# Kernel tuning notes

Hardware: AMD Instinct MI355X
Metric: run time of the kernel (lower is better)

Reference implementation:

```python
import jax, jax.numpy as jnp
import numpy as np

ALPHA = 0.2  # LeakyReLU negative slope


def _gat_layer(h, dst, adj, w, a_in, a_out, b):
    # h: [N, F_in], dst: [N, K] int (edge (i,k): i -> dst[i,k]), adj: [N, K]
    hid = h @ w                      # [N, D]
    s_in = hid @ a_in                # [N]  (attention applied to source-node half)
    s_out = hid @ a_out              # [N]  (attention applied to dest-node half)
    # edge scores, grouped per source node (matches view(-1, num_neighs) softmax)
    e = jax.nn.leaky_relu(s_in[:, None] + s_out[dst], ALPHA)   # [N, K]
    # torch code detaches attention (Variable(..., requires_grad=False))
    att = jax.lax.stop_gradient(jax.nn.softmax(e, axis=1))     # [N, K]
    w_edge = adj * att                                          # [N, K]
    # SpMM: out[i] = sum_k w_edge[i,k] * hid[dst[i,k]]
    out = jnp.einsum('nk,nkd->nd', w_edge, hid[dst]) + b        # [N, D]
    return out


def setup_inputs() -> dict:
    key = jax.random.key(0)
    ks = jax.random.split(key, 12)
    N, K, F, H, O = 100000, 16, 128, 128, 128
    stdv1 = 1.0 / np.sqrt(H)
    stdv2 = 1.0 / np.sqrt(O)
    u = lambda k, shp, s: jax.random.uniform(k, shp, jnp.float32, -s, s)
    return {
        'x': jax.random.normal(ks[0], (N, F), jnp.float32),
        'dst_idx': jax.random.randint(ks[1], (N, K), 0, N),
        'adj_vals': jax.random.uniform(ks[2], (N, K), jnp.float32),
        'w1': u(ks[3], (F, H), stdv1),
        'a_in1': jax.random.normal(ks[4], (H,), jnp.float32) * (1.414 / np.sqrt(H)),
        'a_out1': jax.random.normal(ks[5], (H,), jnp.float32) * (1.414 / np.sqrt(H)),
        'b1': u(ks[6], (H,), stdv1),
        'w2': u(ks[7], (H, O), stdv2),
        'a_in2': jax.random.normal(ks[8], (O,), jnp.float32) * (1.414 / np.sqrt(O)),
        'a_out2': jax.random.normal(ks[9], (O,), jnp.float32) * (1.414 / np.sqrt(O)),
        'b2': u(ks[10], (O,), stdv2),
    }


def reference(x, dst_idx, adj_vals, w1, a_in1, a_out1, b1, w2, a_in2, a_out2, b2):
    h = jax.nn.relu(_gat_layer(x, dst_idx, adj_vals, w1, a_in1, a_out1, b1))
    h = jax.nn.relu(_gat_layer(h, dst_idx, adj_vals, w2, a_in2, a_out2, b2))
    return h
```

## Files before the change

kernel.cpp:

```cpp
#include <hip/hip_runtime.h>

#define ALPHA 0.2f
#define LDA 136

typedef short bf16x8 __attribute__((ext_vector_type(8)));
typedef float f32x4  __attribute__((ext_vector_type(4)));

static __device__ __forceinline__ float bf2f(unsigned short u) {
    union { unsigned int i; float f; } v; v.i = ((unsigned int)u) << 16; return v.f;
}
static __device__ __forceinline__ unsigned short f2bf(float f) {
    union { float f; unsigned int i; } v; v.f = f;
    unsigned int x = v.i;
    return (unsigned short)((x + 0x7fffu + ((x >> 16) & 1u)) >> 16);
}

__global__ __launch_bounds__(128)
void prep_wT_kernel(const float* __restrict__ w1, const float* __restrict__ w2,
                    unsigned short* __restrict__ wT1, unsigned short* __restrict__ wT2)
{
    const int b = blockIdx.x;
    const float* w = (b >> 4) ? w2 : w1;
    unsigned short* wT = (b >> 4) ? wT2 : wT1;
    const int k0 = (b & 15) * 8;
    const int c = threadIdx.x;

    ushort4 u0, u1;
    u0.x = f2bf(w[(k0 + 0) * 128 + c]); u0.y = f2bf(w[(k0 + 1) * 128 + c]);
    u0.z = f2bf(w[(k0 + 2) * 128 + c]); u0.w = f2bf(w[(k0 + 3) * 128 + c]);
    u1.x = f2bf(w[(k0 + 4) * 128 + c]); u1.y = f2bf(w[(k0 + 5) * 128 + c]);
    u1.z = f2bf(w[(k0 + 6) * 128 + c]); u1.w = f2bf(w[(k0 + 7) * 128 + c]);
    *(ushort4*)&wT[c * 128 + k0]     = u0;
    *(ushort4*)&wT[c * 128 + k0 + 4] = u1;
}

__global__ __launch_bounds__(256, 4)
void gemm_score_mfma(const float* __restrict__ src,
                     const unsigned short* __restrict__ wT,
                     const float* __restrict__ a_in,
                     const float* __restrict__ a_out,
                     unsigned short* __restrict__ hid,
                     float* __restrict__ s_in,
                     float* __restrict__ s_out,
                     int n)
{
    __shared__ short Bs[128 * LDA];
    __shared__ float aS[2][128];

    const int tid  = threadIdx.x;
    const int lane = tid & 63;
    const int wv   = tid >> 6;
    const int m    = lane & 15;
    const int q    = lane >> 4;
    const int rbase = blockIdx.x * 64;
    const int row   = rbase + wv * 16 + m;
    const bool rok  = (row < n);

    if (tid < 128) { aS[0][tid] = a_in[tid]; aS[1][tid] = a_out[tid]; }

    bf16x8 aF[4];
    {
        const float* p = &src[(size_t)row * 128 + q * 8];
        #pragma unroll
        for (int ks = 0; ks < 4; ks++) {
            if (rok) {
                float4 v0 = *(const float4*)(p + ks * 32);
                float4 v1 = *(const float4*)(p + ks * 32 + 4);
                bf16x8 a;
                a[0] = (short)f2bf(v0.x); a[1] = (short)f2bf(v0.y);
                a[2] = (short)f2bf(v0.z); a[3] = (short)f2bf(v0.w);
                a[4] = (short)f2bf(v1.x); a[5] = (short)f2bf(v1.y);
                a[6] = (short)f2bf(v1.z); a[7] = (short)f2bf(v1.w);
                aF[ks] = a;
            } else aF[ks] = (bf16x8){0,0,0,0,0,0,0,0};
        }
    }

    #pragma unroll
    for (int i = 0; i < 8; i++) {
        int e = tid + i * 256;
        int nr = e >> 4, j = (e & 15) * 8;
        int4 v = *(const int4*)&wT[nr * 128 + j];
        *(int4*)&Bs[nr * LDA + j] = v;
    }
    __syncthreads();

    f32x4 acc[8];
    #pragma unroll
    for (int t = 0; t < 8; t++) acc[t] = (f32x4){0.f, 0.f, 0.f, 0.f};

    const short* Bbase = &Bs[m * LDA + q * 8];
    #pragma unroll
    for (int ks = 0; ks < 4; ks++) {
        #pragma unroll
        for (int t = 0; t < 8; t++) {
            bf16x8 bF = *(const bf16x8*)(Bbase + t * 16 * LDA + ks * 32);
            acc[t] = __builtin_amdgcn_mfma_f32_16x16x32_bf16(aF[ks], bF, acc[t], 0, 0, 0);
        }
    }

    float pin[4] = {0.f, 0.f, 0.f, 0.f}, pout[4] = {0.f, 0.f, 0.f, 0.f};
    #pragma unroll
    for (int t = 0; t < 8; t++) {
        float ai = aS[0][t * 16 + m];
        float ao = aS[1][t * 16 + m];
        #pragma unroll
        for (int r = 0; r < 4; r++) {
            pin[r]  += acc[t][r] * ai;
            pout[r] += acc[t][r] * ao;
        }
    }
    #pragma unroll
    for (int msk = 8; msk >= 1; msk >>= 1) {
        #pragma unroll
        for (int r = 0; r < 4; r++) {
            pin[r]  += __shfl_xor(pin[r],  msk);
            pout[r] += __shfl_xor(pout[r], msk);
        }
    }
    if (m == 0) {
        #pragma unroll
        for (int r = 0; r < 4; r++) {
            int g = rbase + wv * 16 + q * 4 + r;
            if (g < n) { s_in[g] = pin[r]; s_out[g] = pout[r]; }
        }
    }

    __syncthreads();
    short* Es = Bs;
    #pragma unroll
    for (int t = 0; t < 8; t++)
        #pragma unroll
        for (int r = 0; r < 4; r++)
            Es[(wv * 16 + q * 4 + r) * LDA + t * 16 + m] = (short)f2bf(acc[t][r]);
    __syncthreads();
    #pragma unroll
    for (int i = 0; i < 4; i++) {
        int e = tid + i * 256;
        int r = e >> 4, j = (e & 15) * 8;
        int gr = rbase + r;
        if (gr < n) {
            int4 v = *(const int4*)&Es[r * LDA + j];
            *(int4*)&hid[(size_t)gr * 128 + j] = v;
        }
    }
}

__global__ __launch_bounds__(256, 4)
void fused_agg_gemm(const unsigned short* __restrict__ hid1,
                    const float* __restrict__ s_in1,
                    const float* __restrict__ s_out1,
                    const int* __restrict__ dst,
                    const float* __restrict__ adj,
                    const float* __restrict__ bias1,
                    const unsigned short* __restrict__ wT2,
                    const float* __restrict__ a_in2,
                    const float* __restrict__ a_out2,
                    unsigned short* __restrict__ hid2,
                    float* __restrict__ s_in2,
                    float* __restrict__ s_out2,
                    int n)
{
    __shared__ short As[64 * LDA];
    __shared__ short Bs[64 * LDA];
    __shared__ float aS[2][128];

    const int tid  = threadIdx.x;
    const int lane = tid & 63;
    const int wv   = tid >> 6;
    const int rbase = blockIdx.x * 64;

    if (tid < 128) { aS[0][tid] = a_in2[tid]; aS[1][tid] = a_out2[tid]; }

    #pragma unroll
    for (int i = 0; i < 4; i++) {
        int e = tid + i * 256;
        int nr = e >> 4, j = (e & 15) * 8;
        int4 v = *(const int4*)&wT2[nr * 128 + j];
        *(int4*)&Bs[nr * LDA + j] = v;
    }

    const int jn  = lane >> 2;
    const int kq  = lane & 3;
    const int node = rbase + wv * 16 + jn;
    const bool nok = (node < n);

    int4   dk4 = make_int4(0, 0, 0, 0);
    float4 av4 = make_float4(0.f, 0.f, 0.f, 0.f);
    float  si  = 0.f;
    if (nok) {
        dk4 = *(const int4*)&dst[node * 16 + kq * 4];
        av4 = *(const float4*)&adj[node * 16 + kq * 4];
        si  = s_in1[node];
    }
    float e0 = si + s_out1[dk4.x], e1 = si + s_out1[dk4.y];
    float e2 = si + s_out1[dk4.z], e3 = si + s_out1[dk4.w];
    e0 = (e0 > 0.f) ? e0 : ALPHA * e0;  e1 = (e1 > 0.f) ? e1 : ALPHA * e1;
    e2 = (e2 > 0.f) ? e2 : ALPHA * e2;  e3 = (e3 > 0.f) ? e3 : ALPHA * e3;
    float mx = fmaxf(fmaxf(e0, e1), fmaxf(e2, e3));
    mx = fmaxf(mx, __shfl_xor(mx, 1));
    mx = fmaxf(mx, __shfl_xor(mx, 2));
    float p0 = __expf(e0 - mx), p1 = __expf(e1 - mx);
    float p2 = __expf(e2 - mx), p3 = __expf(e3 - mx);
    float sm = p0 + p1 + p2 + p3;
    sm += __shfl_xor(sm, 1);
    sm += __shfl_xor(sm, 2);
    const float inv = __frcp_rn(sm);
    float4 wk4 = make_float4(av4.x * p0 * inv, av4.y * p1 * inv,
                             av4.z * p2 * inv, av4.w * p3 * inv);

    const int c = lane * 2;
    const float2 bia = *(const float2*)&bias1[c];

    for (int j2 = 0; j2 < 16; j2++) {
        float accx = 0.f, accy = 0.f;
        #pragma unroll
        for (int k = 0; k < 16; k++) {
            const int srcl = j2 * 4 + (k >> 2);
            int   sdk, swki;
            if ((k & 3) == 0) { sdk = __builtin_amdgcn_readlane(dk4.x, srcl);
                                swki = __builtin_amdgcn_readlane(__float_as_int(wk4.x), srcl); }
            else if ((k & 3) == 1) { sdk = __builtin_amdgcn_readlane(dk4.y, srcl);
                                swki = __builtin_amdgcn_readlane(__float_as_int(wk4.y), srcl); }
            else if ((k & 3) == 2) { sdk = __builtin_amdgcn_readlane(dk4.z, srcl);
                                swki = __builtin_amdgcn_readlane(__float_as_int(wk4.z), srcl); }
            else             { sdk = __builtin_amdgcn_readlane(dk4.w, srcl);
                                swki = __builtin_amdgcn_readlane(__float_as_int(wk4.w), srcl); }
            float swk = __int_as_float(swki);
            ushort2 hq = *(const ushort2*)&hid1[(size_t)sdk * 128 + c];
            accx += swk * bf2f(hq.x);
            accy += swk * bf2f(hq.y);
        }
        float ox = fmaxf(accx + bia.x, 0.f);
        float oy = fmaxf(accy + bia.y, 0.f);
        ushort2 hv; hv.x = f2bf(ox); hv.y = f2bf(oy);
        *(ushort2*)&As[(wv * 16 + j2) * LDA + c] = hv;
    }
    __syncthreads();

    const int m = lane & 15;
    const int q = lane >> 4;

    bf16x8 aF[4];
    {
        const short* Abase = &As[(wv * 16 + m) * LDA + q * 8];
        #pragma unroll
        for (int ks = 0; ks < 4; ks++)
            aF[ks] = *(const bf16x8*)(Abase + ks * 32);
    }

    f32x4 acc[8];
    #pragma unroll
    for (int t = 0; t < 8; t++) acc[t] = (f32x4){0.f, 0.f, 0.f, 0.f};

    const short* Bbase = &Bs[m * LDA + q * 8];
    #pragma unroll
    for (int ks = 0; ks < 4; ks++) {
        #pragma unroll
        for (int t = 0; t < 4; t++) {
            bf16x8 bF = *(const bf16x8*)(Bbase + t * 16 * LDA + ks * 32);
            acc[t] = __builtin_amdgcn_mfma_f32_16x16x32_bf16(aF[ks], bF, acc[t], 0, 0, 0);
        }
    }
    __syncthreads();
    #pragma unroll
    for (int i = 0; i < 4; i++) {
        int e = tid + i * 256;
        int nr = e >> 4, j = (e & 15) * 8;
        int4 v = *(const int4*)&wT2[(64 + nr) * 128 + j];
        *(int4*)&Bs[nr * LDA + j] = v;
    }
    __syncthreads();
    #pragma unroll
    for (int ks = 0; ks < 4; ks++) {
        #pragma unroll
        for (int t = 4; t < 8; t++) {
            bf16x8 bF = *(const bf16x8*)(Bbase + (t - 4) * 16 * LDA + ks * 32);
            acc[t] = __builtin_amdgcn_mfma_f32_16x16x32_bf16(aF[ks], bF, acc[t], 0, 0, 0);
        }
    }

    float pin[4] = {0.f, 0.f, 0.f, 0.f}, pout[4] = {0.f, 0.f, 0.f, 0.f};
    #pragma unroll
    for (int t = 0; t < 8; t++) {
        float ai = aS[0][t * 16 + m];
        float ao = aS[1][t * 16 + m];
        #pragma unroll
        for (int r = 0; r < 4; r++) {
            pin[r]  += acc[t][r] * ai;
            pout[r] += acc[t][r] * ao;
        }
    }
    #pragma unroll
    for (int msk = 8; msk >= 1; msk >>= 1) {
        #pragma unroll
        for (int r = 0; r < 4; r++) {
            pin[r]  += __shfl_xor(pin[r],  msk);
            pout[r] += __shfl_xor(pout[r], msk);
        }
    }
    if (m == 0) {
        #pragma unroll
        for (int r = 0; r < 4; r++) {
            int g = rbase + wv * 16 + q * 4 + r;
            if (g < n) { s_in2[g] = pin[r]; s_out2[g] = pout[r]; }
        }
    }

    __syncthreads();
    short* Es = As;
    #pragma unroll
    for (int t = 0; t < 8; t++)
        #pragma unroll
        for (int r = 0; r < 4; r++)
            Es[(wv * 16 + q * 4 + r) * LDA + t * 16 + m] = (short)f2bf(acc[t][r]);
    __syncthreads();
    #pragma unroll
    for (int i = 0; i < 4; i++) {
        int e = tid + i * 256;
        int r = e >> 4, j = (e & 15) * 8;
        int gr = rbase + r;
        if (gr < n) {
            int4 v = *(const int4*)&Es[r * LDA + j];
            *(int4*)&hid2[(size_t)gr * 128 + j] = v;
        }
    }
}

__global__ __launch_bounds__(256)
void gat_aggregate_final(const unsigned short* __restrict__ hid,
                         const float* __restrict__ s_in,
                         const float* __restrict__ s_out,
                         const int* __restrict__ dst,
                         const float* __restrict__ adj,
                         const float* __restrict__ bias,
                         float* __restrict__ out,
                         int n)
{
    const int lane = threadIdx.x & 63;
    const int node = (blockIdx.x * 256 + threadIdx.x) >> 6;
    if (node >= n) return;

    float sc = -1e30f;
    int dk = 0;
    float av = 0.f;
    if (lane < 16) {
        int ei = node * 16 + lane;
        dk = dst[ei];
        av = adj[ei];
        float e = s_in[node] + s_out[dk];
        sc = (e > 0.f) ? e : ALPHA * e;
    }
    float m = sc;
    #pragma unroll
    for (int msk = 8; msk >= 1; msk >>= 1) m = fmaxf(m, __shfl_xor(m, msk));
    float p = (lane < 16) ? __expf(sc - m) : 0.f;
    float s = p;
    #pragma unroll
    for (int msk = 8; msk >= 1; msk >>= 1) s += __shfl_xor(s, msk);
    float wk = (lane < 16) ? av * p / s : 0.f;

    const int c = lane * 2;
    float accx = 0.f, accy = 0.f;
    #pragma unroll
    for (int k = 0; k < 16; k++) {
        int   sdk = __builtin_amdgcn_readlane(dk, k);
        float swk = __int_as_float(__builtin_amdgcn_readlane(__float_as_int(wk), k));
        ushort2 hq = *(const ushort2*)&hid[(size_t)sdk * 128 + c];
        accx += swk * bf2f(hq.x);
        accy += swk * bf2f(hq.y);
    }
    float ox = fmaxf(accx + bias[c],     0.f);
    float oy = fmaxf(accy + bias[c + 1], 0.f);
    *(float2*)&out[(size_t)node * 128 + c] = make_float2(ox, oy);
}

extern "C" void kernel_launch(void* const* d_in, const int* in_sizes, int n_in,
                              void* d_out, int out_size, void* d_ws, size_t ws_size,
                              hipStream_t stream)
{
    const float* x      = (const float*)d_in[0];
    const int*   dst    = (const int*)d_in[1];
    const float* adj    = (const float*)d_in[2];
    const float* w1     = (const float*)d_in[3];
    const float* a_in1  = (const float*)d_in[4];
    const float* a_out1 = (const float*)d_in[5];
    const float* b1     = (const float*)d_in[6];
    const float* w2     = (const float*)d_in[7];
    const float* a_in2  = (const float*)d_in[8];
    const float* a_out2 = (const float*)d_in[9];
    const float* b2     = (const float*)d_in[10];

    const int N = in_sizes[0] / 128;

    unsigned short* hid2  = (unsigned short*)d_ws;
    float*          s_in1 = (float*)(hid2 + (size_t)N * 128);
    float*          s_out1= s_in1 + N;
    float*          s_in2 = s_out1 + N;
    float*          s_out2= s_in2 + N;
    unsigned short* wT1   = (unsigned short*)(s_out2 + N);
    unsigned short* wT2   = wT1 + 128 * 128;
    unsigned short* hid1  = (unsigned short*)d_out + out_size;

    dim3 blk(256);
    dim3 ggrid((N + 63) / 64);
    dim3 agrid((N + 3) / 4);

    prep_wT_kernel<<<32, 128, 0, stream>>>(w1, w2, wT1, wT2);

    gemm_score_mfma<<<ggrid, blk, 0, stream>>>(x, wT1, a_in1, a_out1,
                                               hid1, s_in1, s_out1, N);
    fused_agg_gemm<<<ggrid, blk, 0, stream>>>(hid1, s_in1, s_out1, dst, adj, b1,
                                              wT2, a_in2, a_out2,
                                              hid2, s_in2, s_out2, N);
    gat_aggregate_final<<<agrid, blk, 0, stream>>>(hid2, s_in2, s_out2, dst, adj,
                                                   b2, (float*)d_out, N);
}
```

Measured before the change: 250.3 us.

## Gather neighbor rows with 16-byte loads via LDS edge tables in both aggregations

```diff
diff --git a/kernel.cpp b/kernel.cpp
--- a/kernel.cpp
+++ b/kernel.cpp
@@ -13,6 +13,18 @@
     union { float f; unsigned int i; } v; v.f = f;
     unsigned int x = v.i;
     return (unsigned short)((x + 0x7fffu + ((x >> 16) & 1u)) >> 16);
+}
+static __device__ __forceinline__ float bflo(int u) {
+    union { unsigned int i; float f; } v; v.i = ((unsigned int)u) << 16; return v.f;
+}
+static __device__ __forceinline__ float bfhi(int u) {
+    union { unsigned int i; float f; } v; v.i = ((unsigned int)u) & 0xffff0000u; return v.f;
+}
+static __device__ __forceinline__ void acc8(float* a, const int4 hv, const float w) {
+    a[0] = fmaf(w, bflo(hv.x), a[0]); a[1] = fmaf(w, bfhi(hv.x), a[1]);
+    a[2] = fmaf(w, bflo(hv.y), a[2]); a[3] = fmaf(w, bfhi(hv.y), a[3]);
+    a[4] = fmaf(w, bflo(hv.z), a[4]); a[5] = fmaf(w, bfhi(hv.z), a[5]);
+    a[6] = fmaf(w, bflo(hv.w), a[6]); a[7] = fmaf(w, bfhi(hv.w), a[7]);
 }
 
 __global__ __launch_bounds__(128)
@@ -206,40 +218,52 @@
     sm += __shfl_xor(sm, 1);
     sm += __shfl_xor(sm, 2);
     const float inv = __frcp_rn(sm);
-    float4 wk4 = make_float4(av4.x * p0 * inv, av4.y * p1 * inv,
-                             av4.z * p2 * inv, av4.w * p3 * inv);
-
-    const int c = lane * 2;
-    const float2 bia = *(const float2*)&bias1[c];
-
-    for (int j2 = 0; j2 < 16; j2++) {
-        float accx = 0.f, accy = 0.f;
-        #pragma unroll
-        for (int k = 0; k < 16; k++) {
-            const int srcl = j2 * 4 + (k >> 2);
-            int   sdk, swki;
-            if ((k & 3) == 0) { sdk = __builtin_amdgcn_readlane(dk4.x, srcl);
-                                swki = __builtin_amdgcn_readlane(__float_as_int(wk4.x), srcl); }
-            else if ((k & 3) == 1) { sdk = __builtin_amdgcn_readlane(dk4.y, srcl);
-                                swki = __builtin_amdgcn_readlane(__float_as_int(wk4.y), srcl); }
-            else if ((k & 3) == 2) { sdk = __builtin_amdgcn_readlane(dk4.z, srcl);
-                                swki = __builtin_amdgcn_readlane(__float_as_int(wk4.z), srcl); }
-            else             { sdk = __builtin_amdgcn_readlane(dk4.w, srcl);
-                                swki = __builtin_amdgcn_readlane(__float_as_int(wk4.w), srcl); }
-            float swk = __int_as_float(swki);
-            ushort2 hq = *(const ushort2*)&hid1[(size_t)sdk * 128 + c];
-            accx += swk * bf2f(hq.x);
-            accy += swk * bf2f(hq.y);
-        }
-        float ox = fmaxf(accx + bia.x, 0.f);
-        float oy = fmaxf(accy + bia.y, 0.f);
-        ushort2 hv; hv.x = f2bf(ox); hv.y = f2bf(oy);
-        *(ushort2*)&As[(wv * 16 + j2) * LDA + c] = hv;
-    }
-    __syncthreads();
+
+    {
+        short* rowp = &As[(wv * 16 + jn) * LDA];
+        int4 pa = make_int4(dk4.x, __float_as_int(av4.x * p0 * inv),
+                            dk4.y, __float_as_int(av4.y * p1 * inv));
+        int4 pb = make_int4(dk4.z, __float_as_int(av4.z * p2 * inv),
+                            dk4.w, __float_as_int(av4.w * p3 * inv));
+        *(int4*)(rowp + kq * 16)     = pa;
+        *(int4*)(rowp + kq * 16 + 8) = pb;
+    }
 
     const int m = lane & 15;
     const int q = lane >> 4;
+    {
+        const float4 bb0 = *(const float4*)&bias1[m * 8];
+        const float4 bb1 = *(const float4*)&bias1[m * 8 + 4];
+        #pragma unroll
+        for (int jj = 0; jj < 4; jj++) {
+            const int rloc = wv * 16 + jj * 4 + q;
+            const short* trow = &As[rloc * LDA];
+            float acc[8] = {0.f, 0.f, 0.f, 0.f, 0.f, 0.f, 0.f, 0.f};
+            #pragma unroll
+            for (int k2 = 0; k2 < 8; k2++) {
+                const int4 pp  = *(const int4*)(trow + k2 * 8);
+                const int4 hv0 = *(const int4*)&hid1[((size_t)(unsigned)pp.x << 7) + (m << 3)];
+                const int4 hv1 = *(const int4*)&hid1[((size_t)(unsigned)pp.z << 7) + (m << 3)];
+                acc8(acc, hv0, __int_as_float(pp.y));
+                acc8(acc, hv1, __int_as_float(pp.w));
+            }
+            const float r0 = fmaxf(acc[0] + bb0.x, 0.f);
+            const float r1 = fmaxf(acc[1] + bb0.y, 0.f);
+            const float r2 = fmaxf(acc[2] + bb0.z, 0.f);
+            const float r3 = fmaxf(acc[3] + bb0.w, 0.f);
+            const float r4 = fmaxf(acc[4] + bb1.x, 0.f);
+            const float r5 = fmaxf(acc[5] + bb1.y, 0.f);
+            const float r6 = fmaxf(acc[6] + bb1.z, 0.f);
+            const float r7 = fmaxf(acc[7] + bb1.w, 0.f);
+            int4 ov;
+            ov.x = (int)f2bf(r0) | ((int)f2bf(r1) << 16);
+            ov.y = (int)f2bf(r2) | ((int)f2bf(r3) << 16);
+            ov.z = (int)f2bf(r4) | ((int)f2bf(r5) << 16);
+            ov.w = (int)f2bf(r6) | ((int)f2bf(r7) << 16);
+            *(int4*)&As[rloc * LDA + m * 8] = ov;
+        }
+    }
+    __syncthreads();
 
     bf16x8 aF[4];
     {
@@ -327,7 +351,7 @@
     }
 }
 
-__global__ __launch_bounds__(256)
+__global__ __launch_bounds__(256, 4)
 void gat_aggregate_final(const unsigned short* __restrict__ hid,
                          const float* __restrict__ s_in,
                          const float* __restrict__ s_out,
@@ -337,42 +361,81 @@
                          float* __restrict__ out,
                          int n)
 {
-    const int lane = threadIdx.x & 63;
-    const int node = (blockIdx.x * 256 + threadIdx.x) >> 6;
-    if (node >= n) return;
-
-    float sc = -1e30f;
-    int dk = 0;
-    float av = 0.f;
-    if (lane < 16) {
-        int ei = node * 16 + lane;
-        dk = dst[ei];
-        av = adj[ei];
-        float e = s_in[node] + s_out[dk];
-        sc = (e > 0.f) ? e : ALPHA * e;
-    }
-    float m = sc;
-    #pragma unroll
-    for (int msk = 8; msk >= 1; msk >>= 1) m = fmaxf(m, __shfl_xor(m, msk));
-    float p = (lane < 16) ? __expf(sc - m) : 0.f;
-    float s = p;
-    #pragma unroll
-    for (int msk = 8; msk >= 1; msk >>= 1) s += __shfl_xor(s, msk);
-    float wk = (lane < 16) ? av * p / s : 0.f;
-
-    const int c = lane * 2;
-    float accx = 0.f, accy = 0.f;
-    #pragma unroll
-    for (int k = 0; k < 16; k++) {
-        int   sdk = __builtin_amdgcn_readlane(dk, k);
-        float swk = __int_as_float(__builtin_amdgcn_readlane(__float_as_int(wk), k));
-        ushort2 hq = *(const ushort2*)&hid[(size_t)sdk * 128 + c];
-        accx += swk * bf2f(hq.x);
-        accy += swk * bf2f(hq.y);
-    }
-    float ox = fmaxf(accx + bias[c],     0.f);
-    float oy = fmaxf(accy + bias[c + 1], 0.f);
-    *(float2*)&out[(size_t)node * 128 + c] = make_float2(ox, oy);
+    __shared__ __align__(16) int2 tbl[64][18];
+    const int tid  = threadIdx.x;
+    const int lane = tid & 63;
+    const int wv   = tid >> 6;
+    const int rbase = blockIdx.x * 64;
+
+    const int jn  = lane >> 2;
+    const int kq  = lane & 3;
+    const int node = rbase + wv * 16 + jn;
+    const bool nok = (node < n);
+
+    int4   dk4 = make_int4(0, 0, 0, 0);
+    float4 av4 = make_float4(0.f, 0.f, 0.f, 0.f);
+    float  si  = 0.f;
+    if (nok) {
+        dk4 = *(const int4*)&dst[node * 16 + kq * 4];
+        av4 = *(const float4*)&adj[node * 16 + kq * 4];
+        si  = s_in[node];
+    }
+    float e0 = si + s_out[dk4.x], e1 = si + s_out[dk4.y];
+    float e2 = si + s_out[dk4.z], e3 = si + s_out[dk4.w];
+    e0 = (e0 > 0.f) ? e0 : ALPHA * e0;  e1 = (e1 > 0.f) ? e1 : ALPHA * e1;
+    e2 = (e2 > 0.f) ? e2 : ALPHA * e2;  e3 = (e3 > 0.f) ? e3 : ALPHA * e3;
+    float mx = fmaxf(fmaxf(e0, e1), fmaxf(e2, e3));
+    mx = fmaxf(mx, __shfl_xor(mx, 1));
+    mx = fmaxf(mx, __shfl_xor(mx, 2));
+    float p0 = __expf(e0 - mx), p1 = __expf(e1 - mx);
+    float p2 = __expf(e2 - mx), p3 = __expf(e3 - mx);
+    float sm = p0 + p1 + p2 + p3;
+    sm += __shfl_xor(sm, 1);
+    sm += __shfl_xor(sm, 2);
+    const float inv = __frcp_rn(sm);
+
+    {
+        int4 pa = make_int4(dk4.x, __float_as_int(av4.x * p0 * inv),
+                            dk4.y, __float_as_int(av4.y * p1 * inv));
+        int4 pb = make_int4(dk4.z, __float_as_int(av4.z * p2 * inv),
+                            dk4.w, __float_as_int(av4.w * p3 * inv));
+        *(int4*)&tbl[wv * 16 + jn][kq * 4]     = pa;
+        *(int4*)&tbl[wv * 16 + jn][kq * 4 + 2] = pb;
+    }
+
+    const int m = lane & 15;
+    const int q = lane >> 4;
+    const float4 bb0 = *(const float4*)&bias[m * 8];
+    const float4 bb1 = *(const float4*)&bias[m * 8 + 4];
+
+    #pragma unroll
+    for (int jj = 0; jj < 4; jj++) {
+        const int rl = wv * 16 + jj * 4 + q;
+        const int nodeg = rbase + rl;
+        float acc[8] = {0.f, 0.f, 0.f, 0.f, 0.f, 0.f, 0.f, 0.f};
+        #pragma unroll
+        for (int k2 = 0; k2 < 8; k2++) {
+            const int4 pp  = *(const int4*)&tbl[rl][k2 * 2];
+            const int4 hv0 = *(const int4*)&hid[((size_t)(unsigned)pp.x << 7) + (m << 3)];
+            const int4 hv1 = *(const int4*)&hid[((size_t)(unsigned)pp.z << 7) + (m << 3)];
+            acc8(acc, hv0, __int_as_float(pp.y));
+            acc8(acc, hv1, __int_as_float(pp.w));
+        }
+        if (nodeg < n) {
+            float4 o0, o1;
+            o0.x = fmaxf(acc[0] + bb0.x, 0.f);
+            o0.y = fmaxf(acc[1] + bb0.y, 0.f);
+            o0.z = fmaxf(acc[2] + bb0.z, 0.f);
+            o0.w = fmaxf(acc[3] + bb0.w, 0.f);
+            o1.x = fmaxf(acc[4] + bb1.x, 0.f);
+            o1.y = fmaxf(acc[5] + bb1.y, 0.f);
+            o1.z = fmaxf(acc[6] + bb1.z, 0.f);
+            o1.w = fmaxf(acc[7] + bb1.w, 0.f);
+            float* op = &out[(size_t)nodeg * 128 + m * 8];
+            *(float4*)op       = o0;
+            *(float4*)(op + 4) = o1;
+        }
+    }
 }
 
 extern "C" void kernel_launch(void* const* d_in, const int* in_sizes, int n_in,
@@ -404,7 +467,6 @@
 
     dim3 blk(256);
     dim3 ggrid((N + 63) / 64);
-    dim3 agrid((N + 3) / 4);
 
     prep_wT_kernel<<<32, 128, 0, stream>>>(w1, w2, wT1, wT2);
 
@@ -413,6 +475,6 @@
     fused_agg_gemm<<<ggrid, blk, 0, stream>>>(hid1, s_in1, s_out1, dst, adj, b1,
                                               wT2, a_in2, a_out2,
                                               hid2, s_in2, s_out2, N);
-    gat_aggregate_final<<<agrid, blk, 0, stream>>>(hid2, s_in2, s_out2, dst, adj,
+    gat_aggregate_final<<<ggrid, blk, 0, stream>>>(hid2, s_in2, s_out2, dst, adj,
                                                    b2, (float*)d_out, N);
 }
```

After: 252.4 us. No clear change (+0.8%).
